# Kernel optimization log

Measured on AMD Instinct MI355X. Metric: run time of the kernel, lower is better.

## Reference

```python
import jax, jax.numpy as jnp
import numpy as np

D_MODEL, D_K, D_V, H = 1024, 64, 64, 16


def setup_inputs() -> dict:
    key = jax.random.key(0)
    ks = jax.random.split(key, 11)
    b, nq, nk = 2, 2048, 2048
    queries = jax.random.normal(ks[0], (b, nq, D_MODEL), dtype=jnp.float32)
    keys = jax.random.normal(ks[1], (b, nk, D_MODEL), dtype=jnp.float32)
    values = jax.random.normal(ks[2], (b, nk, D_MODEL), dtype=jnp.float32)
    def xavier(k, shape):
        fan_in, fan_out = shape[1], shape[0]
        lim = np.sqrt(6.0 / (fan_in + fan_out)).astype(np.float32)
        return jax.random.uniform(k, shape, jnp.float32, -lim, lim)
    # torch Linear weight shape: (out_features, in_features)
    Wq = xavier(ks[3], (H * D_K, D_MODEL)); bq = jnp.zeros((H * D_K,), jnp.float32)
    Wk = xavier(ks[4], (H * D_K, D_MODEL)); bk = jnp.zeros((H * D_K,), jnp.float32)
    Wv = xavier(ks[5], (H * D_V, D_MODEL)); bv = jnp.zeros((H * D_V,), jnp.float32)
    Wo = xavier(ks[6], (D_MODEL, H * D_V)); bo = jnp.zeros((D_MODEL,), jnp.float32)
    return {"queries": queries, "keys": keys, "values": values,
            "Wq": Wq, "bq": bq, "Wk": Wk, "bk": bk,
            "Wv": Wv, "bv": bv, "Wo": Wo, "bo": bo}


def reference(queries, keys, values, Wq, bq, Wk, bk, Wv, bv, Wo, bo):
    b, nq, _ = queries.shape
    nk = keys.shape[1]
    scale = 1.0 / np.sqrt(D_K).astype(np.float32)
    # projections -> (b, h, n, d)
    q = (queries @ Wq.T + bq).reshape(b, nq, H, D_K).transpose(0, 2, 1, 3)
    k = (keys @ Wk.T + bk).reshape(b, nk, H, D_K).transpose(0, 2, 1, 3)
    v = (values @ Wv.T + bv).reshape(b, nk, H, D_V).transpose(0, 2, 1, 3)
    att = jnp.einsum('bhqd,bhkd->bhqk', q, k) * scale  # (b,h,nq,nk)
    att = jax.nn.softmax(att, axis=-1)
    out = jnp.einsum('bhqk,bhkd->bhqd', att, v)        # (b,h,nq,dv)
    out = out.transpose(0, 2, 1, 3).reshape(b, nq, H * D_V)
    return out @ Wo.T + bo
```

## Files before the change

### kernel.cpp

```cpp
#include <hip/hip_runtime.h>
#include <stdint.h>

typedef __bf16 v8bf __attribute__((ext_vector_type(8)));
typedef float  v4f  __attribute__((ext_vector_type(4)));

#define QSCALE 0.18033688011112042f

typedef __attribute__((address_space(3))) void lds_vp;
typedef const __attribute__((address_space(1))) void gbl_vp;
__device__ __forceinline__ void gl_lds16(const __bf16* g, __bf16* l) {
    __builtin_amdgcn_global_load_lds((gbl_vp*)g, (lds_vp*)l, 16, 0, 0);
}

__device__ __forceinline__ v8bf cvt8(const float* __restrict__ p) {
    float4 x = *reinterpret_cast<const float4*>(p);
    float4 y = *reinterpret_cast<const float4*>(p + 4);
    v8bf r;
    r[0] = (__bf16)x.x; r[1] = (__bf16)x.y; r[2] = (__bf16)x.z; r[3] = (__bf16)x.w;
    r[4] = (__bf16)y.x; r[5] = (__bf16)y.y; r[6] = (__bf16)y.z; r[7] = (__bf16)y.w;
    return r;
}

__global__ __launch_bounds__(256) void cvt_w(
    const float* __restrict__ w0, const float* __restrict__ w1,
    const float* __restrict__ w2, const float* __restrict__ w3,
    __bf16* __restrict__ o0, __bf16* __restrict__ o1,
    __bf16* __restrict__ o2, __bf16* __restrict__ o3)
{
    const float* src; __bf16* dst;
    switch (blockIdx.y) {
        case 0: src = w0; dst = o0; break;
        case 1: src = w1; dst = o1; break;
        case 2: src = w2; dst = o2; break;
        default: src = w3; dst = o3; break;
    }
    size_t i = ((size_t)blockIdx.x * 256 + threadIdx.x) * 8;
    *reinterpret_cast<v8bf*>(dst + i) = cvt8(src + i);
}

__global__ __launch_bounds__(256) void cvt_in(
    const float* __restrict__ i0, const float* __restrict__ i1,
    const float* __restrict__ i2,
    __bf16* __restrict__ o0, __bf16* __restrict__ o1, __bf16* __restrict__ o2)
{
    const float* src; __bf16* dst;
    switch (blockIdx.y) {
        case 0: src = i0; dst = o0; break;
        case 1: src = i1; dst = o1; break;
        default: src = i2; dst = o2; break;
    }
    size_t i = ((size_t)blockIdx.x * 256 + threadIdx.x) * 8;
    *reinterpret_cast<v8bf*>(dst + i) = cvt8(src + i);
}

__device__ __forceinline__ void gemm_body(
    const __bf16* __restrict__ A, const __bf16* __restrict__ W,
    const float* __restrict__ bias, void* __restrict__ outp,
    int mode, float oscale, int bx, int by)
{
    constexpr int K = 1024, N = 1024;
    __shared__ __align__(16) __bf16 As[2][128 * 64];
    __shared__ __align__(16) __bf16 Bs[2][64 * 64];

    const int lane = threadIdx.x & 63;
    const int wave = threadIdx.x >> 6;
    const int quad = lane >> 4;
    const int l15  = lane & 15;
    const int m_base = bx * 128;
    const int n_base = by * 64;
    const int wm = (wave & 1) * 64;
    const int wn = (wave >> 1) * 32;

    int arow[4], acol[4], brow[2], bcol[2];
    #pragma unroll
    for (int i = 0; i < 4; ++i) {
        int L = (i * 4 + wave) * 64 + lane;
        int r = L >> 3, s = L & 7;
        arow[i] = r; acol[i] = (s ^ (r & 7)) * 8;
    }
    #pragma unroll
    for (int i = 0; i < 2; ++i) {
        int L = (i * 4 + wave) * 64 + lane;
        int r = L >> 3, s = L & 7;
        brow[i] = r; bcol[i] = (s ^ (r & 7)) * 8;
    }

    v4f acc[4][2];
    #pragma unroll
    for (int f = 0; f < 4; ++f)
        #pragma unroll
        for (int g = 0; g < 2; ++g) { v4f z = {0.f,0.f,0.f,0.f}; acc[f][g] = z; }

    #pragma unroll
    for (int i = 0; i < 4; ++i)
        gl_lds16(A + (size_t)(m_base + arow[i]) * K + acol[i],
                 &As[0][(i * 4 + wave) * 512]);
    #pragma unroll
    for (int i = 0; i < 2; ++i)
        gl_lds16(W + (size_t)(n_base + brow[i]) * K + bcol[i],
                 &Bs[0][(i * 4 + wave) * 512]);
    __syncthreads();

    for (int it = 0; it < 16; ++it) {
        const int cur = it & 1, nxt = cur ^ 1;
        const int kn = ((it + 1) & 15) * 64;
        #pragma unroll
        for (int i = 0; i < 4; ++i)
            gl_lds16(A + (size_t)(m_base + arow[i]) * K + kn + acol[i],
                     &As[nxt][(i * 4 + wave) * 512]);
        #pragma unroll
        for (int i = 0; i < 2; ++i)
            gl_lds16(W + (size_t)(n_base + brow[i]) * K + kn + bcol[i],
                     &Bs[nxt][(i * 4 + wave) * 512]);

        #pragma unroll
        for (int ks = 0; ks < 2; ++ks) {
            v8bf af[4], bf[2];
            #pragma unroll
            for (int f = 0; f < 4; ++f) {
                const int R = wm + f * 16 + l15;
                const int slot = (ks * 4 + quad) ^ (R & 7);
                af[f] = *reinterpret_cast<const v8bf*>(&As[cur][R * 64 + slot * 8]);
            }
            #pragma unroll
            for (int g = 0; g < 2; ++g) {
                const int R = wn + g * 16 + l15;
                const int slot = (ks * 4 + quad) ^ (R & 7);
                bf[g] = *reinterpret_cast<const v8bf*>(&Bs[cur][R * 64 + slot * 8]);
            }
            __builtin_amdgcn_s_setprio(1);
            #pragma unroll
            for (int f = 0; f < 4; ++f)
                #pragma unroll
                for (int g = 0; g < 2; ++g)
                    acc[f][g] = __builtin_amdgcn_mfma_f32_16x16x32_bf16(
                        af[f], bf[g], acc[f][g], 0, 0, 0);
            __builtin_amdgcn_s_setprio(0);
        }
        __syncthreads();
    }

    #pragma unroll
    for (int f = 0; f < 4; ++f)
        #pragma unroll
        for (int g = 0; g < 2; ++g) {
            const int nc = n_base + wn + g * 16 + l15;
            const float bval = bias[nc];
            #pragma unroll
            for (int r = 0; r < 4; ++r) {
                const int m = m_base + wm + f * 16 + quad * 4 + r;
                const float v = (acc[f][g][r] + bval) * oscale;
                if (mode == 2) {
                    ((float*)outp)[(size_t)m * N + nc] = v;
                } else {
                    int b = m >> 11, n = m & 2047, h = nc >> 6, d = nc & 63;
                    size_t off = (mode == 0)
                        ? ((size_t)(b * 16 + h) * 2048 + n) * 64 + d
                        : ((size_t)(b * 16 + h) * 64 + d) * 2048 + n;
                    ((__bf16*)outp)[off] = (__bf16)v;
                }
            }
        }
}

__global__ __launch_bounds__(256) void qkv_gemm(
    const __bf16* __restrict__ Aq, const __bf16* __restrict__ Ak,
    const __bf16* __restrict__ Av,
    const __bf16* __restrict__ Wq, const __bf16* __restrict__ Wk,
    const __bf16* __restrict__ Wv,
    const float* __restrict__ bq, const float* __restrict__ bk,
    const float* __restrict__ bv,
    __bf16* __restrict__ Qo, __bf16* __restrict__ Ko, __bf16* __restrict__ Vo)
{
    const int id = blockIdx.x;
    const int by = id & 15;
    const int bx = (id >> 4) & 31;
    const int z  = id >> 9;

    const __bf16 *A, *W; const float* bias; __bf16* outp; float oscale; int mode;
    switch (z) {
        case 0:  A = Aq; W = Wq; bias = bq; outp = Qo; oscale = QSCALE; mode = 0; break;
        case 1:  A = Ak; W = Wk; bias = bk; outp = Ko; oscale = 1.0f;   mode = 0; break;
        default: A = Av; W = Wv; bias = bv; outp = Vo; oscale = 1.0f;   mode = 1; break;
    }
    gemm_body(A, W, bias, outp, mode, oscale, bx, by);
}

__global__ __launch_bounds__(256) void out_gemm(
    const __bf16* __restrict__ A, const __bf16* __restrict__ W,
    const float* __restrict__ bias, float* __restrict__ outp)
{
    const int by = blockIdx.x & 15;
    const int bx = blockIdx.x >> 4;
    gemm_body(A, W, bias, outp, 2, 1.0f, bx, by);
}

__global__ __launch_bounds__(512, 6) void attn_kernel(
    const __bf16* __restrict__ Q, const __bf16* __restrict__ Kb_,
    const __bf16* __restrict__ Vt, __bf16* __restrict__ O)
{
    __shared__ __align__(16) __bf16 Ks[2][64 * 64];
    __shared__ __align__(16) __bf16 Vs[2][64 * 64];
    __shared__ __align__(16) __bf16 p_lds[8][16][72];

    const int lane = threadIdx.x & 63;
    const int wave = threadIdx.x >> 6;
    const int quad = lane >> 4;
    const int l15  = lane & 15;
    const int bh = blockIdx.x & 31;
    const int qt = blockIdx.x >> 5;
    const int b  = bh >> 4, h = bh & 15;

    const __bf16* Qh = Q   + (size_t)bh * 2048 * 64;
    const __bf16* Kh = Kb_ + (size_t)bh * 2048 * 64;
    const __bf16* Vh = Vt  + (size_t)bh * 64 * 2048;

    const int L    = wave * 64 + lane;
    const int srow = L >> 3;
    const int scol = ((L & 7) ^ (srow & 7)) * 8;

    v8bf qf[2];
    #pragma unroll
    for (int ks = 0; ks < 2; ++ks)
        qf[ks] = *reinterpret_cast<const v8bf*>(
            Qh + (size_t)(qt * 128 + wave * 16 + l15) * 64 + ks * 32 + quad * 8);

    v4f o_acc[4];
    #pragma unroll
    for (int c = 0; c < 4; ++c) { v4f z = {0.f,0.f,0.f,0.f}; o_acc[c] = z; }
    float l_r[4] = {0.f, 0.f, 0.f, 0.f};

    gl_lds16(Kh + (size_t)srow * 64 + scol, &Ks[0][L * 8]);
    gl_lds16(Vh + (size_t)srow * 2048 + scol, &Vs[0][L * 8]);
    __syncthreads();

    for (int kt = 0; kt < 32; ++kt) {
        const int cur = kt & 1, nxt = cur ^ 1;
        const int ktn = (kt + 1) & 31;
        gl_lds16(Kh + (size_t)(ktn * 64 + srow) * 64 + scol, &Ks[nxt][L * 8]);
        gl_lds16(Vh + (size_t)srow * 2048 + ktn * 64 + scol, &Vs[nxt][L * 8]);

        v4f s_t[4];
        #pragma unroll
        for (int c = 0; c < 4; ++c) { v4f z = {0.f,0.f,0.f,0.f}; s_t[c] = z; }
        #pragma unroll
        for (int ks = 0; ks < 2; ++ks) {
            v8bf kf[4];
            #pragma unroll
            for (int c = 0; c < 4; ++c) {
                const int R = c * 16 + l15;
                const int slot = (ks * 4 + quad) ^ (R & 7);
                kf[c] = *reinterpret_cast<const v8bf*>(&Ks[cur][R * 64 + slot * 8]);
            }
            __builtin_amdgcn_s_setprio(1);
            #pragma unroll
            for (int c = 0; c < 4; ++c)
                s_t[c] = __builtin_amdgcn_mfma_f32_16x16x32_bf16(qf[ks], kf[c], s_t[c], 0, 0, 0);
            __builtin_amdgcn_s_setprio(0);
        }

        #pragma unroll
        for (int r = 0; r < 4; ++r) {
            const float p0 = __builtin_exp2f(s_t[0][r]);
            const float p1 = __builtin_exp2f(s_t[1][r]);
            const float p2 = __builtin_exp2f(s_t[2][r]);
            const float p3 = __builtin_exp2f(s_t[3][r]);
            l_r[r] += (p0 + p1) + (p2 + p3);
            p_lds[wave][quad * 4 + r][0 * 16 + l15] = (__bf16)p0;
            p_lds[wave][quad * 4 + r][1 * 16 + l15] = (__bf16)p1;
            p_lds[wave][quad * 4 + r][2 * 16 + l15] = (__bf16)p2;
            p_lds[wave][quad * 4 + r][3 * 16 + l15] = (__bf16)p3;
        }

        #pragma unroll
        for (int ks = 0; ks < 2; ++ks) {
            v8bf vf[4];
            #pragma unroll
            for (int c = 0; c < 4; ++c) {
                const int R = c * 16 + l15;
                const int slot = (ks * 4 + quad) ^ (R & 7);
                vf[c] = *reinterpret_cast<const v8bf*>(&Vs[cur][R * 64 + slot * 8]);
            }
            const v8bf pf = *reinterpret_cast<const v8bf*>(
                &p_lds[wave][l15][ks * 32 + quad * 8]);
            __builtin_amdgcn_s_setprio(1);
            #pragma unroll
            for (int c = 0; c < 4; ++c)
                o_acc[c] = __builtin_amdgcn_mfma_f32_16x16x32_bf16(pf, vf[c], o_acc[c], 0, 0, 0);
            __builtin_amdgcn_s_setprio(0);
        }
        __syncthreads();
    }

    #pragma unroll
    for (int r = 0; r < 4; ++r) {
        float l = l_r[r];
        #pragma unroll
        for (int off = 1; off < 16; off <<= 1)
            l += __shfl_xor(l, off, 16);
        const float inv_l = 1.0f / l;
        const int qr = qt * 128 + wave * 16 + quad * 4 + r;
        #pragma unroll
        for (int c = 0; c < 4; ++c) {
            const int col = h * 64 + c * 16 + l15;
            O[(size_t)(b * 2048 + qr) * 1024 + col] = (__bf16)(o_acc[c][r] * inv_l);
        }
    }
}

extern "C" void kernel_launch(void* const* d_in, const int* in_sizes, int n_in,
                              void* d_out, int out_size, void* d_ws, size_t ws_size,
                              hipStream_t stream) {
    const float* q_in = (const float*)d_in[0];
    const float* k_in = (const float*)d_in[1];
    const float* v_in = (const float*)d_in[2];
    const float* Wq = (const float*)d_in[3];
    const float* bq = (const float*)d_in[4];
    const float* Wk = (const float*)d_in[5];
    const float* bk = (const float*)d_in[6];
    const float* Wv = (const float*)d_in[7];
    const float* bv = (const float*)d_in[8];
    const float* Wo = (const float*)d_in[9];
    const float* bo = (const float*)d_in[10];
    float* out = (float*)d_out;

    __bf16* ws  = (__bf16*)d_ws;
    __bf16* Abq = ws;
    __bf16* Abk = Abq + 4194304;
    __bf16* Abv = Abk + 4194304;
    __bf16* Qb  = Abv + 4194304;
    __bf16* Kb  = Qb  + 4194304;
    __bf16* Vb  = Kb  + 4194304;
    __bf16* Wqb = Vb  + 4194304;
    __bf16* Wkb = Wqb + 1048576;
    __bf16* Wvb = Wkb + 1048576;
    __bf16* Wob = Wvb + 1048576;
    __bf16* Ob  = Abq;

    cvt_w<<<dim3(512, 4), 256, 0, stream>>>(Wq, Wk, Wv, Wo, Wqb, Wkb, Wvb, Wob);
    cvt_in<<<dim3(2048, 3), 256, 0, stream>>>(q_in, k_in, v_in, Abq, Abk, Abv);

    qkv_gemm<<<1536, 256, 0, stream>>>(
        Abq, Abk, Abv, Wqb, Wkb, Wvb, bq, bk, bv, Qb, Kb, Vb);

    attn_kernel<<<512, 512, 0, stream>>>(Qb, Kb, Vb, Ob);

    out_gemm<<<512, 256, 0, stream>>>(Ob, Wob, bo, out);
}
```

Measured before the change: 248.3 us.

## Load K/V fragments directly from global memory instead of LDS staging

Removes the double-buffered LDS staging of K and V tiles and the per-iteration block barrier. Each wave now loads its K and V MFMA fragments straight from global memory into registers, relying on L1/L2 cache for reuse across the 8 waves. The occupancy hint drops from 6 to 4 blocks per CU to leave room for the extra fragment registers. This trades LDS traffic and synchronisation for redundant global/cache loads and longer load latency with no explicit prefetch.

```diff
diff --git a/kernel.cpp b/kernel.cpp
--- a/kernel.cpp
+++ b/kernel.cpp
@@ -195,12 +195,10 @@
     gemm_body(A, W, bias, outp, 2, 1.0f, bx, by);
 }
 
-__global__ __launch_bounds__(512, 6) void attn_kernel(
+__global__ __launch_bounds__(512, 4) void attn_kernel(
     const __bf16* __restrict__ Q, const __bf16* __restrict__ Kb_,
     const __bf16* __restrict__ Vt, __bf16* __restrict__ O)
 {
-    __shared__ __align__(16) __bf16 Ks[2][64 * 64];
-    __shared__ __align__(16) __bf16 Vs[2][64 * 64];
     __shared__ __align__(16) __bf16 p_lds[8][16][72];
 
     const int lane = threadIdx.x & 63;
@@ -215,10 +213,6 @@
     const __bf16* Kh = Kb_ + (size_t)bh * 2048 * 64;
     const __bf16* Vh = Vt  + (size_t)bh * 64 * 2048;
 
-    const int L    = wave * 64 + lane;
-    const int srow = L >> 3;
-    const int scol = ((L & 7) ^ (srow & 7)) * 8;
-
     v8bf qf[2];
     #pragma unroll
     for (int ks = 0; ks < 2; ++ks)
@@ -230,32 +224,31 @@
     for (int c = 0; c < 4; ++c) { v4f z = {0.f,0.f,0.f,0.f}; o_acc[c] = z; }
     float l_r[4] = {0.f, 0.f, 0.f, 0.f};
 
-    gl_lds16(Kh + (size_t)srow * 64 + scol, &Ks[0][L * 8]);
-    gl_lds16(Vh + (size_t)srow * 2048 + scol, &Vs[0][L * 8]);
-    __syncthreads();
-
     for (int kt = 0; kt < 32; ++kt) {
-        const int cur = kt & 1, nxt = cur ^ 1;
-        const int ktn = (kt + 1) & 31;
-        gl_lds16(Kh + (size_t)(ktn * 64 + srow) * 64 + scol, &Ks[nxt][L * 8]);
-        gl_lds16(Vh + (size_t)srow * 2048 + ktn * 64 + scol, &Vs[nxt][L * 8]);
+        v8bf kf[2][4];
+        #pragma unroll
+        for (int ks = 0; ks < 2; ++ks)
+            #pragma unroll
+            for (int c = 0; c < 4; ++c)
+                kf[ks][c] = *reinterpret_cast<const v8bf*>(
+                    Kh + (size_t)(kt * 64 + c * 16 + l15) * 64 + ks * 32 + quad * 8);
+        v8bf vf[2][4];
+        #pragma unroll
+        for (int ks = 0; ks < 2; ++ks)
+            #pragma unroll
+            for (int c = 0; c < 4; ++c)
+                vf[ks][c] = *reinterpret_cast<const v8bf*>(
+                    Vh + (size_t)(c * 16 + l15) * 2048 + kt * 64 + ks * 32 + quad * 8);
 
         v4f s_t[4];
         #pragma unroll
         for (int c = 0; c < 4; ++c) { v4f z = {0.f,0.f,0.f,0.f}; s_t[c] = z; }
         #pragma unroll
         for (int ks = 0; ks < 2; ++ks) {
-            v8bf kf[4];
-            #pragma unroll
-            for (int c = 0; c < 4; ++c) {
-                const int R = c * 16 + l15;
-                const int slot = (ks * 4 + quad) ^ (R & 7);
-                kf[c] = *reinterpret_cast<const v8bf*>(&Ks[cur][R * 64 + slot * 8]);
-            }
             __builtin_amdgcn_s_setprio(1);
             #pragma unroll
             for (int c = 0; c < 4; ++c)
-                s_t[c] = __builtin_amdgcn_mfma_f32_16x16x32_bf16(qf[ks], kf[c], s_t[c], 0, 0, 0);
+                s_t[c] = __builtin_amdgcn_mfma_f32_16x16x32_bf16(qf[ks], kf[ks][c], s_t[c], 0, 0, 0);
             __builtin_amdgcn_s_setprio(0);
         }
 
@@ -274,22 +267,14 @@
 
         #pragma unroll
         for (int ks = 0; ks < 2; ++ks) {
-            v8bf vf[4];
-            #pragma unroll
-            for (int c = 0; c < 4; ++c) {
-                const int R = c * 16 + l15;
-                const int slot = (ks * 4 + quad) ^ (R & 7);
-                vf[c] = *reinterpret_cast<const v8bf*>(&Vs[cur][R * 64 + slot * 8]);
-            }
             const v8bf pf = *reinterpret_cast<const v8bf*>(
                 &p_lds[wave][l15][ks * 32 + quad * 8]);
             __builtin_amdgcn_s_setprio(1);
             #pragma unroll
             for (int c = 0; c < 4; ++c)
-                o_acc[c] = __builtin_amdgcn_mfma_f32_16x16x32_bf16(pf, vf[c], o_acc[c], 0, 0, 0);
+                o_acc[c] = __builtin_amdgcn_mfma_f32_16x16x32_bf16(pf, vf[ks][c], o_acc[c], 0, 0, 0);
             __builtin_amdgcn_s_setprio(0);
         }
-        __syncthreads();
     }
 
     #pragma unroll
```

New measurement: 407.3 us. +64.1%, slower.
